# Kernel optimization log

Hardware: AMD Instinct MI355X
Metric: run time of the kernel (lower is better)

## Reference

```python
import jax, jax.numpy as jnp
import numpy as np

# dims
B, T, E = 2, 4096, 512
H = 8
DH = E // H            # 64 per-head dim
DEPTH = 4
NHASH = 4              # n_hashes
BUCKET = 64            # bucket_size
NB = T // BUCKET       # n_buckets = 64 (even)
VOCAB, NCLASS = 32000, 10
FF = 4 * E
MASK_VAL = -1e9        # causal mask value
SELF_VAL = -5e4        # TOKEN_SELF_ATTN_VALUE


def layer_norm(x, g, b):
    m = jnp.mean(x, axis=-1, keepdims=True)
    v = jnp.var(x, axis=-1, keepdims=True)
    return (x - m) * jax.lax.rsqrt(v + 1e-5) * g + b


def lsh_attention(x, wqk, wv, wo, bo, rot):
    """Reformer LSH causal self-attention (eval mode, shared QK, n_hashes rounds)."""
    qk = (x @ wqk).reshape(B, T, H, DH).transpose(0, 2, 1, 3).reshape(B * H, T, DH)
    v = (x @ wv).reshape(B, T, H, DH).transpose(0, 2, 1, 3).reshape(B * H, T, DH)
    b = B * H
    # --- hash: random rotations -> bucket ids per hash round ---
    rotated = jnp.einsum('btf,fhi->bhti', qk, rot)             # (b, NHASH, T, NB//2)
    rotated = jnp.concatenate([rotated, -rotated], axis=-1)    # (b, NHASH, T, NB)
    buckets = jnp.argmax(rotated, axis=-1)                     # (b, NHASH, T)
    buckets = buckets + (jnp.arange(NHASH) * NB)[None, :, None]
    buckets = buckets.reshape(b, NHASH * T)
    # --- stable sort by (bucket, time) ---
    ticker = jnp.arange(NHASH * T)
    bt = buckets * T + (ticker % T)
    sticker = jnp.argsort(bt, axis=-1)                         # sort permutation
    undo_sort = jnp.argsort(sticker, axis=-1)
    st = sticker % T                                           # original time index of sorted slot
    sqk = jnp.take_along_axis(qk, st[..., None], axis=1)
    sv = jnp.take_along_axis(v, st[..., None], axis=1)
    # --- chunk into buckets, attend to own + previous chunk ---
    C = NHASH * NB                                             # number of chunks
    bq_t = st.reshape(b, C, BUCKET)
    bqk = sqk.reshape(b, C, BUCKET, DH)
    bv = sv.reshape(b, C, BUCKET, DH)
    bq = bqk
    bk = bqk / jnp.maximum(jnp.linalg.norm(bqk, axis=-1, keepdims=True), 1e-12)
    look = lambda t: jnp.concatenate([t, jnp.roll(t, 1, axis=1)], axis=2)
    bk, bvl, bkv_t = look(bk), look(bv), look(bq_t)
    dots = jnp.einsum('bcie,bcje->bcij', bq, bk) * (DH ** -0.5)  # (b, C, BUCKET, 2*BUCKET)
    causal = bq_t[:, :, :, None] < bkv_t[:, :, None, :]
    dots = jnp.where(causal, MASK_VAL, dots)
    self_m = bq_t[:, :, :, None] == bkv_t[:, :, None, :]
    dots = jnp.where(self_m, SELF_VAL, dots)
    lse = jax.nn.logsumexp(dots, axis=-1, keepdims=True)
    probs = jnp.exp(dots - lse)
    so = jnp.einsum('bcij,bcje->bcie', probs, bvl).reshape(b, NHASH * T, DH)
    slogits = lse.reshape(b, NHASH * T)
    # --- unsort and combine hash rounds via logsumexp weights ---
    o = jnp.take_along_axis(so, undo_sort[..., None], axis=1).reshape(b, NHASH, T, DH)
    logits = jnp.take_along_axis(slogits, undo_sort, axis=1).reshape(b, NHASH, T, 1)
    w = jnp.exp(logits - jax.nn.logsumexp(logits, axis=1, keepdims=True))
    out = jnp.sum(o * w, axis=1)                               # (b, T, DH)
    out = out.reshape(B, H, T, DH).transpose(0, 2, 1, 3).reshape(B, T, E)
    return out @ wo + bo


def feed_forward(x, w1, b1, w2, b2):
    return jax.nn.gelu(x @ w1 + b1, approximate=False) @ w2 + b2


def setup_inputs() -> dict:
    key = jax.random.key(0)
    ks = jax.random.split(key, 12)
    n = lambda k, s: (0.02 * jax.random.normal(k, s)).astype(jnp.float32)
    return {
        'x': jax.random.randint(ks[0], (B, T), 0, VOCAB),
        'tok_emb': n(ks[1], (VOCAB, E)),
        'pos_emb': n(ks[2], (T, E)),
        'rotations': jax.random.normal(ks[3], (DEPTH, DH, NHASH, NB // 2), dtype=jnp.float32),
        'ln1_g': jnp.ones((DEPTH, E), jnp.float32), 'ln1_b': jnp.zeros((DEPTH, E), jnp.float32),
        'w_qk': n(ks[4], (DEPTH, E, E)), 'w_v': n(ks[5], (DEPTH, E, E)),
        'w_o': n(ks[6], (DEPTH, E, E)), 'b_o': jnp.zeros((DEPTH, E), jnp.float32),
        'ln2_g': jnp.ones((DEPTH, E), jnp.float32), 'ln2_b': jnp.zeros((DEPTH, E), jnp.float32),
        'w_ff1': n(ks[7], (DEPTH, E, FF)), 'b_ff1': jnp.zeros((DEPTH, FF), jnp.float32),
        'w_ff2': n(ks[8], (DEPTH, FF, E)), 'b_ff2': jnp.zeros((DEPTH, E), jnp.float32),
        'w_final': n(ks[9], (E, NCLASS)), 'b_final': jnp.zeros((NCLASS,), jnp.float32),
    }


def reference(x, tok_emb, pos_emb, rotations, ln1_g, ln1_b, w_qk, w_v, w_o, b_o,
              ln2_g, ln2_b, w_ff1, b_ff1, w_ff2, b_ff2, w_final, b_final):
    h = tok_emb[x] + pos_emb[None, :, :]
    # reversible sequence: y1 = x1 + attn(ln(x2)); y2 = x2 + ff(ln(y1))
    x1, x2 = h, h
    for d in range(DEPTH):
        x1 = x1 + lsh_attention(layer_norm(x2, ln1_g[d], ln1_b[d]),
                                w_qk[d], w_v[d], w_o[d], b_o[d], rotations[d])
        x2 = x2 + feed_forward(layer_norm(x1, ln2_g[d], ln2_b[d]),
                               w_ff1[d], b_ff1[d], w_ff2[d], b_ff2[d])
    h = 0.5 * (x1 + x2)
    pooled = jnp.mean(h, axis=1)          # pooling == 'avg'
    return pooled @ w_final + b_final
```

## Files before the change

### kernel.cpp

```cpp
#include <hip/hip_runtime.h>
#include <hip/hip_bf16.h>
#include <math.h>

#define B_      2
#define T_      4096
#define E_      512
#define H_      8
#define DH_     64
#define DEPTH_  4
#define NHASH_  4
#define BUCKET_ 64
#define NB_     64
#define NB2_    32
#define C_      (NHASH_*NB_)
#define BH_     (B_*H_)
#define NT_     (NHASH_*T_)
#define FF_     2048
#define NCLASS_ 10
#define MASKV   (-1e9f)
#define SELFV   (-5e4f)

typedef __attribute__((ext_vector_type(8))) short short8;
typedef __attribute__((ext_vector_type(4))) float f32x4;

__device__ __forceinline__ void gload_lds16(const void* g, void* l) {
    __builtin_amdgcn_global_load_lds(
        (const __attribute__((address_space(1))) void*)g,
        (__attribute__((address_space(3))) void*)l,
        16, 0, 0);
}

__device__ __forceinline__ unsigned pk2(float a, float b) {
    __hip_bfloat16 ha = __float2bfloat16(a), hb = __float2bfloat16(b);
    unsigned short ua = *(unsigned short*)&ha, ub = *(unsigned short*)&hb;
    return (unsigned)ua | ((unsigned)ub << 16);
}

__global__ __launch_bounds__(128) void k_embed(const int* __restrict__ x, const float* __restrict__ tok,
                                               const float* __restrict__ pos, float* __restrict__ x1,
                                               float* __restrict__ x2)
{
    int bt = blockIdx.x;
    int t  = bt & (T_ - 1);
    int id = x[bt];
    float4 tv = ((const float4*)(tok + (size_t)id * E_))[threadIdx.x];
    float4 pv = ((const float4*)(pos + (size_t)t * E_))[threadIdx.x];
    float4 hv = make_float4(tv.x + pv.x, tv.y + pv.y, tv.z + pv.z, tv.w + pv.w);
    ((float4*)(x1 + (size_t)bt * E_))[threadIdx.x] = hv;
    ((float4*)(x2 + (size_t)bt * E_))[threadIdx.x] = hv;
}

template<bool LO>
__global__ __launch_bounds__(128) void k_ln(const float* __restrict__ in, const float* __restrict__ g,
                                            const float* __restrict__ b, __hip_bfloat16* __restrict__ out,
                                            __hip_bfloat16* __restrict__ outlo)
{
    int row = blockIdx.x, tid = threadIdx.x;
    float4 v = ((const float4*)(in + (size_t)row * E_))[tid];
    float s = v.x + v.y + v.z + v.w;
    float q = v.x * v.x + v.y * v.y + v.z * v.z + v.w * v.w;
#pragma unroll
    for (int d = 1; d < 64; d <<= 1) { s += __shfl_xor(s, d); q += __shfl_xor(q, d); }
    __shared__ float red[4];
    int w = tid >> 6;
    if ((tid & 63) == 0) { red[w * 2] = s; red[w * 2 + 1] = q; }
    __syncthreads();
    s = red[0] + red[2]; q = red[1] + red[3];
    float mean = s * (1.0f / E_);
    float var  = q * (1.0f / E_) - mean * mean;
    float rstd = rsqrtf(var + 1e-5f);
    float4 gv = ((const float4*)g)[tid];
    float4 bv = ((const float4*)b)[tid];
    float o0 = (v.x - mean) * rstd * gv.x + bv.x;
    float o1 = (v.y - mean) * rstd * gv.y + bv.y;
    float o2 = (v.z - mean) * rstd * gv.z + bv.z;
    float o3 = (v.w - mean) * rstd * gv.w + bv.w;
    __hip_bfloat16* op = out + (size_t)row * E_ + tid * 4;
    __hip_bfloat16 h0 = __float2bfloat16(o0), h1 = __float2bfloat16(o1);
    __hip_bfloat16 h2 = __float2bfloat16(o2), h3 = __float2bfloat16(o3);
    op[0] = h0; op[1] = h1; op[2] = h2; op[3] = h3;
    if (LO) {
        __hip_bfloat16* lp = outlo + (size_t)row * E_ + tid * 4;
        lp[0] = __float2bfloat16(o0 - __bfloat162float(h0));
        lp[1] = __float2bfloat16(o1 - __bfloat162float(h1));
        lp[2] = __float2bfloat16(o2 - __bfloat162float(h2));
        lp[3] = __float2bfloat16(o3 - __bfloat162float(h3));
    }
}

template<bool SPLIT>
__global__ __launch_bounds__(256) void k_wprep(const float* __restrict__ W, __hip_bfloat16* __restrict__ WT,
                                               __hip_bfloat16* __restrict__ WTlo, int K, int N)
{
    __shared__ float tile[32][33];
    size_t lofs = (size_t)blockIdx.z * K * N;
    W  += lofs;
    WT += lofs;
    if (SPLIT) WTlo += lofs;
    int n0 = blockIdx.x * 32, k0 = blockIdx.y * 32;
    int tx = threadIdx.x & 31, ty = threadIdx.x >> 5;
#pragma unroll
    for (int i = 0; i < 4; ++i) {
        int k = ty + i * 8;
        tile[k][tx] = W[(size_t)(k0 + k) * N + n0 + tx];
    }
    __syncthreads();
#pragma unroll
    for (int i = 0; i < 4; ++i) {
        int n = ty + i * 8;
        float v = tile[tx][n];
        __hip_bfloat16 hv = __float2bfloat16(v);
        WT[(size_t)(n0 + n) * K + k0 + tx] = hv;
        if (SPLIT)
            WTlo[(size_t)(n0 + n) * K + k0 + tx] = __float2bfloat16(v - __bfloat162float(hv));
    }
}

__global__ __launch_bounds__(256) void k_rotprep(const float* __restrict__ rot,
                                                 __hip_bfloat16* __restrict__ rhs,
                                                 __hip_bfloat16* __restrict__ rls)
{
    int d = blockIdx.x;
    rot += (size_t)d * 64 * 128;
    rhs += (size_t)d * 8192;
    rls += (size_t)d * 8192;
    int tid = threadIdx.x;
    for (int idx = tid; idx < 128 * 64; idx += 256) {
        int row = idx >> 6, f = idx & 63;
        float v = rot[(size_t)f * 128 + row];
        __hip_bfloat16 hv = __float2bfloat16(v);
        __hip_bfloat16 lv = __float2bfloat16(v - __bfloat162float(hv));
        int b = f >> 3;
        int off = row * 64 + (((b ^ (row & 7)) << 3) | (f & 7));
        rhs[off] = hv;
        rls[off] = lv;
    }
}

__device__ __forceinline__ float geluf(float x) {
    float ax = fabsf(x) * 0.70710678118654752f;
    float t  = __builtin_amdgcn_rcpf(1.0f + 0.3275911f * ax);
    float poly = t * (0.254829592f + t * (-0.284496736f + t * (1.421413741f +
                 t * (-1.453152027f + t * 1.061405429f))));
    float e = __expf(-ax * ax);
    float erfax = 1.0f - poly * e;
    float erfx = copysignf(erfax, x);
    return 0.5f * x * (1.0f + erfx);
}

template<int OUTK, int BIAS, int TM>
__global__ __launch_bounds__(256) void k_mgemm(const __hip_bfloat16* __restrict__ A,
                                               const __hip_bfloat16* __restrict__ WT,
                                               const float* __restrict__ bias, void* __restrict__ Cout,
                                               int N, int K, int nbnShift)
{
    constexpr int MF = TM / 32;
    constexpr int ABYTES = TM * 128;
    __shared__ __align__(16) char smem[2 * ABYTES + 32768];
    char* BbBase = smem + 2 * ABYTES;

    int tid = threadIdx.x;
    int lane = tid & 63, wv = tid >> 6, w = wv;
    int nwg = gridDim.x;
    int bid = blockIdx.x;
    int swz = (bid & 7) * (nwg >> 3) + (bid >> 3);
    int nmask = (1 << nbnShift) - 1;
    int m0 = (swz >> nbnShift) * TM, n0 = (swz & nmask) * 128;
    int wm = (w >> 1) * (TM / 2), wn = (w & 1) * 64;

    const __hip_bfloat16* aSg[MF];
    int aDd[MF];
#pragma unroll
    for (int g = 0; g < MF; ++g) {
        int d = (wv + g * 4) * 64 + lane;
        int row = d >> 3, slot = d & 7;
        int c = (slot - ((row >> 1) & 7)) & 7;
        aSg[g] = A + (size_t)(m0 + row) * K + c * 8;
        aDd[g] = d * 16;
    }
    const __hip_bfloat16* bSg[4];
    int bDd[4];
#pragma unroll
    for (int g = 0; g < 4; ++g) {
        int d = (wv + g * 4) * 64 + lane;
        int row = d >> 3, slot = d & 7;
        int c = (slot - ((row >> 1) & 7)) & 7;
        bSg[g] = WT + (size_t)(n0 + row) * K + c * 8;
        bDd[g] = d * 16;
    }

    int cch = lane >> 4;
    int aoff[MF][2], boff[4][2];
#pragma unroll
    for (int f = 0; f < MF; ++f) {
        int ar = wm + f * 16 + (lane & 15);
        int rot = (ar >> 1) & 7;
#pragma unroll
        for (int h = 0; h < 2; ++h)
            aoff[f][h] = ar * 128 + (((h * 4 + cch) + rot) & 7) * 16;
    }
#pragma unroll
    for (int f = 0; f < 4; ++f) {
        int br = wn + f * 16 + (lane & 15);
        int rot = (br >> 1) & 7;
#pragma unroll
        for (int h = 0; h < 2; ++h)
            boff[f][h] = br * 128 + (((h * 4 + cch) + rot) & 7) * 16;
    }

    f32x4 acc[MF][4];
#pragma unroll
    for (int i = 0; i < MF; ++i)
#pragma unroll
        for (int j = 0; j < 4; ++j) acc[i][j] = (f32x4){0.f, 0.f, 0.f, 0.f};

    const int NS = K >> 6;
    {
#pragma unroll
        for (int g = 0; g < MF; ++g) gload_lds16(aSg[g], smem + aDd[g]);
#pragma unroll
        for (int g = 0; g < 4; ++g)  gload_lds16(bSg[g], BbBase + bDd[g]);
    }
    __syncthreads();
    for (int s = 0; s < NS; ++s) {
        int cur = s & 1;
        if (s + 1 < NS) {
            int nb = cur ^ 1;
            int kk = (s + 1) * 64;
            char* Abn = smem + nb * ABYTES;
            char* Bbn = BbBase + nb * 16384;
#pragma unroll
            for (int g = 0; g < MF; ++g) gload_lds16(aSg[g] + kk, Abn + aDd[g]);
#pragma unroll
            for (int g = 0; g < 4; ++g)  gload_lds16(bSg[g] + kk, Bbn + bDd[g]);
        }
        const char* Ab = smem + cur * ABYTES;
        const char* Bb = BbBase + cur * 16384;
#pragma unroll
        for (int h = 0; h < 2; ++h) {
            short8 af[MF], bfr[4];
#pragma unroll
            for (int f = 0; f < MF; ++f) af[f] = *(const short8*)(Ab + aoff[f][h]);
#pragma unroll
            for (int f = 0; f < 4; ++f)  bfr[f] = *(const short8*)(Bb + boff[f][h]);
#pragma unroll
            for (int i = 0; i < MF; ++i)
#pragma unroll
                for (int j = 0; j < 4; ++j)
                    acc[i][j] = __builtin_amdgcn_mfma_f32_16x16x32_bf16(af[i], bfr[j], acc[i][j], 0, 0, 0);
        }
        __syncthreads();
    }

    int g = lane >> 4;
    if (OUTK == 2 || OUTK == 3) {
        unsigned short* Ot = (unsigned short*)smem;
#pragma unroll
        for (int i = 0; i < MF; ++i) {
#pragma unroll
            for (int j = 0; j < 4; ++j) {
                int col = wn + j * 16 + (lane & 15);
                float bv = BIAS ? bias[n0 + col] : 0.f;
#pragma unroll
                for (int q = 0; q < 4; ++q) {
                    int row = wm + i * 16 + g * 4 + q;
                    float vv = acc[i][j][q] + bv;
                    if (OUTK == 2) vv = geluf(vv);
                    __hip_bfloat16 hv = __float2bfloat16(vv);
                    Ot[row * 128 + (((col >> 3) ^ (row & 7)) << 3) + (col & 7)] = *(unsigned short*)&hv;
                }
            }
        }
        __syncthreads();
#pragma unroll
        for (int u = 0; u < TM / 16; ++u) {
            int f = u * 256 + tid;
            int row = f >> 4, cblk = f & 15;
            uint4 v = *(const uint4*)(Ot + row * 128 + ((cblk ^ (row & 7)) << 3));
            if (OUTK == 2) {
                *(uint4*)((__hip_bfloat16*)Cout + (size_t)(m0 + row) * N + n0 + cblk * 8) = v;
            } else {
                int mrow = m0 + row;
                int t = mrow & (T_ - 1), bI = mrow >> 12;
                int col = n0 + cblk * 8;
                int h = col >> 6, fin = col & 63;
                *(uint4*)((__hip_bfloat16*)Cout + ((size_t)(bI * H_ + h) * T_ + t) * 64 + fin) = v;
            }
        }
    } else {
        float* Ot = (float*)smem;
        float* Cb = (float*)Cout;
#pragma unroll
        for (int i = 0; i < MF; ++i) {
#pragma unroll
            for (int j = 0; j < 4; ++j) {
                int col = wn + j * 16 + (lane & 15);
#pragma unroll
                for (int q = 0; q < 4; ++q) {
                    int row = wm + i * 16 + g * 4 + q;
                    Ot[row * 128 + (((col >> 2) ^ (row & 7)) << 2) + (col & 3)] = acc[i][j][q];
                }
            }
        }
        __syncthreads();
#pragma unroll
        for (int u = 0; u < 8; ++u) {
            int f = u * 256 + tid;
            int row = f >> 5, c4 = f & 31;
            float4 v = *(const float4*)(Ot + row * 128 + ((c4 ^ (row & 7)) << 2));
            if (BIAS) {
                float4 bv = *(const float4*)(bias + n0 + c4 * 4);
                v.x += bv.x; v.y += bv.y; v.z += bv.z; v.w += bv.w;
            }
            float* cp = Cb + (size_t)(m0 + row) * N + n0 + c4 * 4;
            float4 old = *(const float4*)cp;
            v.x += old.x; v.y += old.y; v.z += old.z; v.w += old.w;
            *(float4*)cp = v;
        }
    }
}

#define STG_A(buf, kt, h) \
    gload_lds16(aSrc + (size_t)((h) * 128) * K + (kt) * 64,      smem + (buf) * 32768 + (h) * 16384 + tid * 16); \
    gload_lds16(aSrc + (size_t)((h) * 128 + 64) * K + (kt) * 64, smem + (buf) * 32768 + (h) * 16384 + 8192 + tid * 16);
#define STG_B(buf, kt, h) \
    gload_lds16(bSrc + (size_t)((h) * 128) * K + (kt) * 64,      smem + 65536 + (buf) * 32768 + (h) * 16384 + tid * 16); \
    gload_lds16(bSrc + (size_t)((h) * 128 + 64) * K + (kt) * 64, smem + 65536 + (buf) * 32768 + (h) * 16384 + 8192 + tid * 16);

#define PHASE8(buf, MH, NH, RA, RB, STAGE, GATE) do {                                             \
    const char* Ab_ = smem + (buf) * 32768;                                                       \
    const char* Bb_ = smem + 65536 + (buf) * 32768;                                               \
    STAGE                                                                                         \
    if (RA) {                                                                                     \
        _Pragma("unroll")                                                                         \
        for (int mf = 0; mf < 4; ++mf) {                                                          \
            int row = arow + (MH) * 128 + mf * 16;                                                \
            aF[mf][0] = *(const short8*)(Ab_ + row * 128 + sw0);                                  \
            aF[mf][1] = *(const short8*)(Ab_ + row * 128 + sw1);                                  \
        }                                                                                         \
    }                                                                                             \
    if (RB) {                                                                                     \
        _Pragma("unroll")                                                                         \
        for (int nf = 0; nf < 2; ++nf) {                                                          \
            int row = brow + (NH) * 128 + nf * 16;                                                \
            bF[nf][0] = *(const short8*)(Bb_ + row * 128 + sw0);                                  \
            bF[nf][1] = *(const short8*)(Bb_ + row * 128 + sw1);                                  \
        }                                                                                         \
    }                                                                                             \
    GATE                                                                                          \
    __builtin_amdgcn_s_barrier();                                                                 \
    asm volatile("s_waitcnt lgkmcnt(0)" ::: "memory");                                            \
    __builtin_amdgcn_sched_barrier(0);                                                            \
    __builtin_amdgcn_s_setprio(1);                                                                \
    _Pragma("unroll")                                                                             \
    for (int mf = 0; mf < 4; ++mf)                                                                \
        _Pragma("unroll")                                                                         \
        for (int nf = 0; nf < 2; ++nf) {                                                          \
            acc[MH][NH][mf][nf] = __builtin_amdgcn_mfma_f32_16x16x32_bf16(aF[mf][0], bF[nf][0], acc[MH][NH][mf][nf], 0, 0, 0); \
            acc[MH][NH][mf][nf] = __builtin_amdgcn_mfma_f32_16x16x32_bf16(aF[mf][1], bF[nf][1], acc[MH][NH][mf][nf], 0, 0, 0); \
        }                                                                                         \
    __builtin_amdgcn_s_setprio(0);                                                                \
    __builtin_amdgcn_s_barrier();                                                                 \
} while (0)

__global__ __launch_bounds__(512, 2) void k_gemm256_gelu(const __hip_bfloat16* __restrict__ A,
                                                         const __hip_bfloat16* __restrict__ WT,
                                                         const float* __restrict__ bias,
                                                         __hip_bfloat16* __restrict__ Cout,
                                                         int N, int K, int nShift)
{
    __shared__ __align__(16) char smem[131072];
    const int NT = K >> 6;
    int tid = threadIdx.x;
    int lane = tid & 63, w = tid >> 6;
    int lane7 = lane & 7, cch = lane >> 4;
    int nwg = gridDim.x;
    int bid = blockIdx.x;
    int swz = (bid & 7) * (nwg >> 3) + (bid >> 3);
    int m0 = (swz >> nShift) * 256;
    int n0 = (swz & ((1 << nShift) - 1)) * 256;

    int rstg = tid >> 3;
    int kcstg = (tid & 7) ^ (rstg & 7);
    const __hip_bfloat16* aSrc = A  + (size_t)(m0 + rstg) * K + kcstg * 8;
    const __hip_bfloat16* bSrc = WT + (size_t)(n0 + rstg) * K + kcstg * 8;

    int arow = (w >> 2) * 64 + (lane & 15);
    int brow = (w & 3) * 32 + (lane & 15);
    int sw0 = (cch ^ lane7) << 4;
    int sw1 = ((4 + cch) ^ lane7) << 4;

    f32x4 acc[2][2][4][2];
#pragma unroll
    for (int a2 = 0; a2 < 2; ++a2)
#pragma unroll
        for (int b2 = 0; b2 < 2; ++b2)
#pragma unroll
            for (int c2 = 0; c2 < 4; ++c2)
#pragma unroll
                for (int d2 = 0; d2 < 2; ++d2) acc[a2][b2][c2][d2] = (f32x4){0.f, 0.f, 0.f, 0.f};

    short8 aF[4][2], bF[2][2];

    STG_A(0, 0, 0) STG_A(0, 0, 1) STG_B(0, 0, 0) STG_B(0, 0, 1)
    if (NT > 1) { STG_A(1, 1, 0) STG_B(1, 1, 1) }
    if (NT > 1) asm volatile("s_waitcnt vmcnt(4)" ::: "memory");
    else        asm volatile("s_waitcnt vmcnt(0)" ::: "memory");
    __builtin_amdgcn_s_barrier();

    for (int t = 0; t < NT; ++t) {
        int buf = t & 1;
        PHASE8(buf, 0, 0, 1, 1, { if (t + 1 < NT) { STG_A(buf ^ 1, t + 1, 1) } }, {});
        PHASE8(buf, 0, 1, 0, 1, { if (t + 1 < NT) { STG_B(buf ^ 1, t + 1, 0) } }, {});
        PHASE8(buf, 1, 1, 1, 0, { if (t + 2 < NT) { STG_A(buf, t + 2, 0) } }, {});
        PHASE8(buf, 1, 0, 0, 1, { if (t + 2 < NT) { STG_B(buf, t + 2, 1) } },
               { if (t + 2 < NT)      asm volatile("s_waitcnt vmcnt(4)" ::: "memory");
                 else if (t + 1 < NT) asm volatile("s_waitcnt vmcnt(0)" ::: "memory"); });
    }

    unsigned short* Ot = (unsigned short*)smem;
    int g = lane >> 4;
#pragma unroll
    for (int mh = 0; mh < 2; ++mh)
#pragma unroll
        for (int nh = 0; nh < 2; ++nh)
#pragma unroll
            for (int nf = 0; nf < 2; ++nf) {
                int coll = nh * 128 + (w & 3) * 32 + nf * 16 + (lane & 15);
                float bv = bias[n0 + coll];
#pragma unroll
                for (int mf = 0; mf < 4; ++mf)
#pragma unroll
                    for (int q = 0; q < 4; ++q) {
                        int rowl = mh * 128 + (w >> 2) * 64 + mf * 16 + g * 4 + q;
                        float vv = geluf(acc[mh][nh][mf][nf][q] + bv);
                        __hip_bfloat16 hv = __float2bfloat16(vv);
                        Ot[rowl * 256 + ((((coll >> 4) ^ (rowl & 7)) << 4) | (coll & 15))] = *(unsigned short*)&hv;
                    }
            }
    __syncthreads();
#pragma unroll
    for (int u = 0; u < 16; ++u) {
        int f = u * 512 + tid;
        int rowl = f >> 5, c16 = f & 31;
        uint4 v = *(const uint4*)(Ot + rowl * 256 + ((((c16 >> 1) ^ (rowl & 7)) << 4) | ((c16 & 1) << 3)));
        *(uint4*)(Cout + (size_t)(m0 + rowl) * N + n0 + c16 * 8) = v;
    }
}
#undef PHASE8
#undef STG_A
#undef STG_B

__global__ __launch_bounds__(256) void k_mgemm_qk(const __hip_bfloat16* __restrict__ Ah,
                                                  const __hip_bfloat16* __restrict__ Al,
                                                  const __hip_bfloat16* __restrict__ Bh,
                                                  const __hip_bfloat16* __restrict__ Bl,
                                                  float* __restrict__ Cout)
{
    __shared__ __align__(16) char smem[49152];
    const int N = 512, K = 512;
    int tid = threadIdx.x;
    int lane = tid & 63, w = tid >> 6;
    int nwg = gridDim.x;
    int bid = blockIdx.x;
    int swz = (bid & 7) * (nwg >> 3) + (bid >> 3);
    int m0 = (swz >> 2) * 64, n0 = (swz & 3) * 128;
    int wm = (w >> 1) * 32, wn = (w & 1) * 64;

    int r0 = tid >> 2, s0 = tid & 3;
    int c0 = (s0 - (r0 >> 1)) & 3;
    int r1 = r0 + 64;
    int c1 = (s0 - (r1 >> 1)) & 3;
    const __hip_bfloat16* ahS  = Ah + (size_t)(m0 + r0) * K + c0 * 8;
    const __hip_bfloat16* alS  = Al + (size_t)(m0 + r0) * K + c0 * 8;
    const __hip_bfloat16* bhS0 = Bh + (size_t)(n0 + r0) * K + c0 * 8;
    const __hip_bfloat16* bhS1 = Bh + (size_t)(n0 + r1) * K + c1 * 8;
    const __hip_bfloat16* blS0 = Bl + (size_t)(n0 + r0) * K + c0 * 8;
    const __hip_bfloat16* blS1 = Bl + (size_t)(n0 + r1) * K + c1 * 8;

    int cch = lane >> 4;
    int aoff[2], boff[4];
#pragma unroll
    for (int f = 0; f < 2; ++f) {
        int ar = wm + f * 16 + (lane & 15);
        aoff[f] = ar * 32 + (((cch + (ar >> 1)) & 3) * 8);
    }
#pragma unroll
    for (int f = 0; f < 4; ++f) {
        int br = wn + f * 16 + (lane & 15);
        boff[f] = br * 32 + (((cch + (br >> 1)) & 3) * 8);
    }

    f32x4 acc[2][4];
#pragma unroll
    for (int i = 0; i < 2; ++i)
#pragma unroll
        for (int j = 0; j < 4; ++j) acc[i][j] = (f32x4){0.f, 0.f, 0.f, 0.f};

#define QK_STAGE(buf, kk)                                                     \
    { char* bb = smem + (buf) * 24576;                                        \
      gload_lds16(ahS  + (kk), bb + tid * 16);                                \
      gload_lds16(alS  + (kk), bb + 4096  + tid * 16);                        \
      gload_lds16(bhS0 + (kk), bb + 8192  + tid * 16);                        \
      gload_lds16(bhS1 + (kk), bb + 12288 + tid * 16);                        \
      gload_lds16(blS0 + (kk), bb + 16384 + tid * 16);                        \
      gload_lds16(blS1 + (kk), bb + 20480 + tid * 16); }

    QK_STAGE(0, 0)
    __syncthreads();
    const int NS = K >> 5;
    for (int s = 0; s < NS; ++s) {
        int cur = s & 1;
        if (s + 1 < NS) QK_STAGE(cur ^ 1, (s + 1) * 32)
        const __hip_bfloat16* AhB = (const __hip_bfloat16*)(smem + cur * 24576);
        const __hip_bfloat16* AlB = (const __hip_bfloat16*)(smem + cur * 24576 + 4096);
        const __hip_bfloat16* BhB = (const __hip_bfloat16*)(smem + cur * 24576 + 8192);
        const __hip_bfloat16* BlB = (const __hip_bfloat16*)(smem + cur * 24576 + 16384);
        short8 afh[2], afl[2], bfh[4], bfl[4];
#pragma unroll
        for (int f = 0; f < 2; ++f) {
            afh[f] = *(const short8*)(AhB + aoff[f]);
            afl[f] = *(const short8*)(AlB + aoff[f]);
        }
#pragma unroll
        for (int f = 0; f < 4; ++f) {
            bfh[f] = *(const short8*)(BhB + boff[f]);
            bfl[f] = *(const short8*)(BlB + boff[f]);
        }
#pragma unroll
        for (int i = 0; i < 2; ++i)
#pragma unroll
            for (int j = 0; j < 4; ++j) {
                acc[i][j] = __builtin_amdgcn_mfma_f32_16x16x32_bf16(afh[i], bfh[j], acc[i][j], 0, 0, 0);
                acc[i][j] = __builtin_amdgcn_mfma_f32_16x16x32_bf16(afh[i], bfl[j], acc[i][j], 0, 0, 0);
                acc[i][j] = __builtin_amdgcn_mfma_f32_16x16x32_bf16(afl[i], bfh[j], acc[i][j], 0, 0, 0);
            }
        __syncthreads();
    }
#undef QK_STAGE

    int g = lane >> 4;
    float* Ot = (float*)smem;
#pragma unroll
    for (int i = 0; i < 2; ++i) {
#pragma unroll
        for (int j = 0; j < 4; ++j) {
            int col = wn + j * 16 + (lane & 15);
#pragma unroll
            for (int q = 0; q < 4; ++q) {
                int row = wm + i * 16 + g * 4 + q;
                Ot[row * 128 + (((col >> 2) ^ (row & 7)) << 2) + (col & 3)] = acc[i][j][q];
            }
        }
    }
    __syncthreads();
#pragma unroll
    for (int u = 0; u < 8; ++u) {
        int f = u * 256 + tid;
        int row = f >> 5, c4 = f & 31;
        float4 v = *(const float4*)(Ot + row * 128 + ((c4 ^ (row & 7)) << 2));
        *(float4*)(Cout + (size_t)(m0 + row) * N + n0 + c4 * 4) = v;
    }
}

__global__ __launch_bounds__(256) void k_hash(const float* __restrict__ qk,
                                              const __hip_bfloat16* __restrict__ rhs,
                                              const __hip_bfloat16* __restrict__ rls,
                                              unsigned char* __restrict__ bkt,
                                              __hip_bfloat16* __restrict__ qh,
                                              __hip_bfloat16* __restrict__ kh)
{
    __shared__ __align__(16) char smem[65536];
    char* RH = smem;
    char* RL = smem + 16384;
    char* QH = smem + 32768;
    char* QL = smem + 49152;
    int tid = threadIdx.x, lane = tid & 63, wv = tid >> 6;
    int bh = blockIdx.x, tc = blockIdx.y;
    int bI = bh >> 3, h = bh & 7;

#pragma unroll
    for (int it = 0; it < 4; ++it) {
        gload_lds16((const char*)rhs + it * 4096 + tid * 16, RH + it * 4096 + tid * 16);
        gload_lds16((const char*)rls + it * 4096 + tid * 16, RL + it * 4096 + tid * 16);
    }

    {
        int t = tid >> 1, half = tid & 1;
        int tg = tc * 128 + t;
        const float4* qsrc = (const float4*)(qk + ((size_t)(bI * T_ + tg)) * E_ + h * DH_ + half * 32);
        float4 q4[8];
        float n2 = 0.f;
#pragma unroll
        for (int j = 0; j < 8; ++j) {
            q4[j] = qsrc[j];
            n2 += q4[j].x * q4[j].x + q4[j].y * q4[j].y + q4[j].z * q4[j].z + q4[j].w * q4[j].w;
        }
        n2 += __shfl_xor(n2, 1);
        float sc = 0.125f / fmaxf(sqrtf(n2), 1e-12f);
        float qv[32];
#pragma unroll
        for (int j = 0; j < 8; ++j) {
            qv[4 * j] = q4[j].x; qv[4 * j + 1] = q4[j].y; qv[4 * j + 2] = q4[j].z; qv[4 * j + 3] = q4[j].w;
        }
        unsigned short hb[32], lb[32], kb[32];
#pragma unroll
        for (int j = 0; j < 32; ++j) {
            __hip_bfloat16 hv = __float2bfloat16(qv[j]);
            __hip_bfloat16 lv = __float2bfloat16(qv[j] - __bfloat162float(hv));
            __hip_bfloat16 kv = __float2bfloat16(qv[j] * sc);
            hb[j] = *(unsigned short*)&hv; lb[j] = *(unsigned short*)&lv; kb[j] = *(unsigned short*)&kv;
        }
        size_t ro = ((size_t)bh * T_ + tg) * 64 + half * 32;
        uint4* qdst = (uint4*)(qh + ro);
        uint4* kdst = (uint4*)(kh + ro);
#pragma unroll
        for (int j = 0; j < 4; ++j) {
            qdst[j] = *(uint4*)&hb[8 * j];
            kdst[j] = *(uint4*)&kb[8 * j];
        }
#pragma unroll
        for (int j = 0; j < 4; ++j) {
            int b = half * 4 + j;
            int xo = t * 128 + ((b ^ (t & 7)) << 4);
            *(uint4*)(QH + xo) = *(uint4*)&hb[8 * j];
            *(uint4*)(QL + xo) = *(uint4*)&lb[8 * j];
        }
    }
    __syncthreads();

#pragma unroll
    for (int sub = 0; sub < 2; ++sub) {
        int tl = wv * 32 + sub * 16 + (lane & 15);
        int g = lane >> 4;
        short8 qfh0 = *(const short8*)(QH + tl * 128 + ((g ^ (tl & 7)) << 4));
        short8 qfh1 = *(const short8*)(QH + tl * 128 + (((4 + g) ^ (tl & 7)) << 4));
        short8 qfl0 = *(const short8*)(QL + tl * 128 + ((g ^ (tl & 7)) << 4));
        short8 qfl1 = *(const short8*)(QL + tl * 128 + (((4 + g) ^ (tl & 7)) << 4));
        f32x4 sacc[8];
#pragma unroll
        for (int kt = 0; kt < 8; ++kt) sacc[kt] = (f32x4){0.f, 0.f, 0.f, 0.f};
#pragma unroll
        for (int kt = 0; kt < 8; ++kt) {
            int row = kt * 16 + (lane & 15);
            short8 rh0 = *(const short8*)(RH + row * 128 + ((g ^ (row & 7)) << 4));
            short8 rh1 = *(const short8*)(RH + row * 128 + (((4 + g) ^ (row & 7)) << 4));
            short8 rl0 = *(const short8*)(RL + row * 128 + ((g ^ (row & 7)) << 4));
            short8 rl1 = *(const short8*)(RL + row * 128 + (((4 + g) ^ (row & 7)) << 4));
            sacc[kt] = __builtin_amdgcn_mfma_f32_16x16x32_bf16(rh0, qfh0, sacc[kt], 0, 0, 0);
            sacc[kt] = __builtin_amdgcn_mfma_f32_16x16x32_bf16(rh1, qfh1, sacc[kt], 0, 0, 0);
            sacc[kt] = __builtin_amdgcn_mfma_f32_16x16x32_bf16(rl0, qfh0, sacc[kt], 0, 0, 0);
            sacc[kt] = __builtin_amdgcn_mfma_f32_16x16x32_bf16(rl1, qfh1, sacc[kt], 0, 0, 0);
            sacc[kt] = __builtin_amdgcn_mfma_f32_16x16x32_bf16(rh0, qfl0, sacc[kt], 0, 0, 0);
            sacc[kt] = __builtin_amdgcn_mfma_f32_16x16x32_bf16(rh1, qfl1, sacc[kt], 0, 0, 0);
        }
#pragma unroll
        for (int rd = 0; rd < 4; ++rd) {
            float bv = -3.0e38f; int bi = 0;
#pragma unroll
            for (int kp = 0; kp < 2; ++kp) {
#pragma unroll
                for (int rr = 0; rr < 4; ++rr) {
                    int i = kp * 16 + g * 4 + rr;
                    float v = sacc[rd * 2 + kp][rr];
                    if (v > bv) { bv = v; bi = i; }
                }
            }
#pragma unroll
            for (int kp = 0; kp < 2; ++kp) {
#pragma unroll
                for (int rr = 0; rr < 4; ++rr) {
                    int i = 32 + kp * 16 + g * 4 + rr;
                    float v = -sacc[rd * 2 + kp][rr];
                    if (v > bv) { bv = v; bi = i; }
                }
            }
#pragma unroll
            for (int dlt = 16; dlt <= 32; dlt <<= 1) {
                float ov = __shfl_xor(bv, dlt);
                int oi = __shfl_xor(bi, dlt);
                if (ov > bv || (ov == bv && oi < bi)) { bv = ov; bi = oi; }
            }
            if (g == 0)
                bkt[((size_t)(bh * NHASH_ + rd)) * T_ + tc * 128 + tl] = (unsigned char)bi;
        }
    }
}

__global__ __launch_bounds__(256) void k_sort(const unsigned char* __restrict__ bkt, int* __restrict__ st)
{
    __shared__ unsigned char bktL[T_];
    __shared__ unsigned short hist[256][66];
    __shared__ unsigned short qtot[4][64];
    __shared__ int qbase[4][64];
    int tid = threadIdx.x;
    int bhr = blockIdx.x;
    const unsigned char* src = bkt + (size_t)bhr * T_;
    ((uint4*)bktL)[tid] = ((const uint4*)src)[tid];
    uint4* h4 = (uint4*)&hist[0][0];
    for (int j = tid; j < 2112; j += 256) h4[j] = make_uint4(0, 0, 0, 0);
    __syncthreads();
    int base = tid * 16;
#pragma unroll
    for (int i = 0; i < 16; ++i) hist[tid][bktL[base + i]]++;
    __syncthreads();
    int b = tid & 63, qd = tid >> 6;
    int t0 = qd * 64;
    unsigned run = 0;
#pragma unroll 8
    for (int tt = 0; tt < 64; ++tt) {
        unsigned v = hist[t0 + tt][b];
        hist[t0 + tt][b] = (unsigned short)run;
        run += v;
    }
    qtot[qd][b] = (unsigned short)run;
    __syncthreads();
    if (tid < 64) {
        int c0 = qtot[0][tid], c1 = qtot[1][tid], c2 = qtot[2][tid], c3 = qtot[3][tid];
        int tot = c0 + c1 + c2 + c3;
        int pre = tot;
#pragma unroll
        for (int d = 1; d < 64; d <<= 1) { int o = __shfl_up(pre, d); if (tid >= d) pre += o; }
        int startb = pre - tot;
        qbase[0][tid] = startb;
        qbase[1][tid] = startb + c0;
        qbase[2][tid] = startb + c0 + c1;
        qbase[3][tid] = startb + c0 + c1 + c2;
    }
    __syncthreads();
    int* dst = st + (size_t)bhr * T_;
#pragma unroll
    for (int i = 0; i < 16; ++i) {
        int bb = bktL[base + i];
        int off = hist[tid][bb]++;
        dst[qbase[qd][bb] + off] = base + i;
    }
}

__global__ __launch_bounds__(256, 2) void k_attn(const __hip_bfloat16* __restrict__ qh,
                                                 const __hip_bfloat16* __restrict__ kh,
                                                 const __hip_bfloat16* __restrict__ vh,
                                                 const int* __restrict__ st,
                                                 __hip_bfloat16* __restrict__ o,
                                                 float* __restrict__ lg)
{
    __shared__ __align__(16) char smem[49664];
    char* KbB = smem;
    char* VtB = smem + 16384;
    char* PbB = smem + 32768;
    int*  kvt = (int*)(smem + 49152);
    unsigned short* ObU = (unsigned short*)smem;

    int tid = threadIdx.x;
    int lane = tid & 63;
    int g = lane >> 4;
    int wv = tid >> 6;
    int wq0 = wv * 16;

    int bid = blockIdx.x;
    int bh = ((bid & 7) << 1) | ((bid >> 3) & 1);
    int c  = bid >> 4;
    int rnd = c >> 6;
    int cp = (c + C_ - 1) & (C_ - 1);
    const size_t stB = (size_t)bh * NT_;

    if (tid < 128) {
        int cc = (tid < 64) ? c : cp;
        kvt[tid] = st[stB + (size_t)cc * 64 + (tid & 63)];
    }
    __syncthreads();

    {
        int k = tid >> 1, half = tid & 1;
        const uint4* src = (const uint4*)(kh + ((size_t)bh * T_ + kvt[k]) * 64 + half * 32);
#pragma unroll
        for (int j2 = 0; j2 < 4; ++j2) {
            uint4 a = src[j2];
            int blk = (half * 4 + j2) ^ (k & 7);
            *(uint4*)(KbB + k * 128 + blk * 16) = a;
        }
    }
    {
        int kp = tid & 63, dq = tid >> 6;
        const uint4* r0 = (const uint4*)(vh + ((size_t)bh * T_ + kvt[2 * kp]) * 64 + dq * 16);
        const uint4* r1 = (const uint4*)(vh + ((size_t)bh * T_ + kvt[2 * kp + 1]) * 64 + dq * 16);
        unsigned short va[16], vb2[16];
        *(uint4*)&va[0] = r0[0];  *(uint4*)&va[8] = r0[1];
        *(uint4*)&vb2[0] = r1[0]; *(uint4*)&vb2[8] = r1[1];
#pragma unroll
        for (int i = 0; i < 16; ++i) {
            int d = dq * 16 + i;
            unsigned wrd = (unsigned)va[i] | ((unsigned)vb2[i] << 16);
            *(unsigned*)(VtB + d * 256 + ((((kp >> 2) ^ i)) << 4) + ((kp & 3) << 2)) = wrd;
        }
    }
    int tq = kvt[wq0 + (lane & 15)];
    const __hip_bfloat16* qrow = qh + ((size_t)bh * T_ + tq) * 64;
    short8 qf0 = *(const short8*)(qrow + g * 8);
    short8 qf1 = *(const short8*)(qrow + 32 + g * 8);
    __syncthreads();

    f32x4 sacc[8];
#pragma unroll
    for (int kt = 0; kt < 8; ++kt) sacc[kt] = (f32x4){0.f, 0.f, 0.f, 0.f};
#pragma unroll
    for (int kt = 0; kt < 8; ++kt) {
        int row = kt * 16 + (lane & 15);
        short8 kf0 = *(const short8*)(KbB + row * 128 + (((g) ^ (row & 7)) << 4));
        short8 kf1 = *(const short8*)(KbB + row * 128 + (((4 + g) ^ (row & 7)) << 4));
        sacc[kt] = __builtin_amdgcn_mfma_f32_16x16x32_bf16(kf0, qf0, sacc[kt], 0, 0, 0);
        sacc[kt] = __builtin_amdgcn_mfma_f32_16x16x32_bf16(kf1, qf1, sacc[kt], 0, 0, 0);
    }

    float m = -3.0e38f;
#pragma unroll
    for (int kt = 0; kt < 8; ++kt) {
#pragma unroll
        for (int r = 0; r < 4; ++r) {
            int tk = kvt[kt * 16 + g * 4 + r];
            float dd = sacc[kt][r];
            dd = (tk > tq) ? MASKV : dd;
            dd = (tk == tq) ? SELFV : dd;
            sacc[kt][r] = dd;
            m = fmaxf(m, dd);
        }
    }
    m = fmaxf(m, __shfl_xor(m, 16));
    m = fmaxf(m, __shfl_xor(m, 32));
    float ssum = 0.f;
#pragma unroll
    for (int kt = 0; kt < 8; ++kt) {
        float p0 = __expf(sacc[kt][0] - m);
        float p1 = __expf(sacc[kt][1] - m);
        float p2 = __expf(sacc[kt][2] - m);
        float p3 = __expf(sacc[kt][3] - m);
        ssum += (p0 + p1) + (p2 + p3);
        uint2 wrd = make_uint2(pk2(p0, p1), pk2(p2, p3));
        int blk = (kt * 2 + (g >> 1)) ^ (lane & 15);
        *(uint2*)(PbB + (wq0 + (lane & 15)) * 256 + (blk << 4) + ((g & 1) << 3)) = wrd;
    }
    ssum += __shfl_xor(ssum, 16);
    ssum += __shfl_xor(ssum, 32);
    if (lane < 16)
        lg[((size_t)bh * T_ + tq) * 4 + rnd] = m + __logf(ssum);

    f32x4 pacc[4];
#pragma unroll
    for (int dt = 0; dt < 4; ++dt) pacc[dt] = (f32x4){0.f, 0.f, 0.f, 0.f};
#pragma unroll
    for (int s = 0; s < 4; ++s) {
        int xr = ((s * 4 + g) ^ (lane & 15)) << 4;
        short8 pf = *(const short8*)(PbB + (wq0 + (lane & 15)) * 256 + xr);
#pragma unroll
        for (int dt = 0; dt < 4; ++dt) {
            short8 vf = *(const short8*)(VtB + (dt * 16 + (lane & 15)) * 256 + xr);
            pacc[dt] = __builtin_amdgcn_mfma_f32_16x16x32_bf16(pf, vf, pacc[dt], 0, 0, 0);
        }
    }
    __syncthreads();

#pragma unroll
    for (int r = 0; r < 4; ++r) {
        float sr = __shfl(ssum, g * 4 + r);
        float inv = 1.0f / sr;
        int rowl = wq0 + g * 4 + r;
#pragma unroll
        for (int dt = 0; dt < 4; ++dt) {
            __hip_bfloat16 hv = __float2bfloat16(pacc[dt][r] * inv);
            ObU[rowl * 72 + dt * 16 + (lane & 15)] = *(unsigned short*)&hv;
        }
    }
    __syncthreads();

    {
        int rr = tid >> 2, seg = tid & 3;
        uint4 a = *(const uint4*)(ObU + rr * 72 + seg * 16);
        uint4 b = *(const uint4*)(ObU + rr * 72 + seg * 16 + 8);
        size_t jor = (size_t)bh * T_ + kvt[rr];
        uint4* dst = (uint4*)(o + jor * 256 + rnd * 64 + seg * 16);
        dst[0] = a; dst[1] = b;
    }
}

__global__ __launch_bounds__(256) void k_combine(const __hip_bfloat16* __restrict__ o,
                                                 const float* __restrict__ lg,
                                                 __hip_bfloat16* __restrict__ att)
{
    __shared__ float ws[H_][8];
    int bt = blockIdx.x;
    int bI = bt >> 12;
    int t  = bt & (T_ - 1);
    int tid = threadIdx.x;
    if (tid < H_) {
        size_t base = ((size_t)(bI * H_ + tid) * T_ + t);
        float4 L = *(const float4*)(lg + base * 4);
        float M = fmaxf(fmaxf(L.x, L.y), fmaxf(L.z, L.w));
        float w0 = __expf(L.x - M), w1 = __expf(L.y - M), w2 = __expf(L.z - M), w3 = __expf(L.w - M);
        float inv = 1.0f / (w0 + w1 + w2 + w3);
        ws[tid][0] = w0 * inv; ws[tid][1] = w1 * inv; ws[tid][2] = w2 * inv; ws[tid][3] = w3 * inv;
    }
    __syncthreads();
#pragma unroll
    for (int it = 0; it < 2; ++it) {
        int e = it * 256 + tid;
        int h = e >> 6, f = e & 63;
        const __hip_bfloat16* op = o + ((size_t)(bI * H_ + h) * T_ + t) * 256;
        float val = __bfloat162float(op[f])       * ws[h][0]
                  + __bfloat162float(op[64 + f])  * ws[h][1]
                  + __bfloat162float(op[128 + f]) * ws[h][2]
                  + __bfloat162float(op[192 + f]) * ws[h][3];
        att[(size_t)bt * E_ + e] = __float2bfloat16(val);
    }
}

__global__ __launch_bounds__(256) void k_pool1(const float* __restrict__ x1, const float* __restrict__ x2,
                                               float* __restrict__ part)
{
    int blk = blockIdx.x;
    int bI = blk >> 5, tc = blk & 31;
    int t0 = tc * 128;
    for (int e = threadIdx.x; e < E_; e += 256) {
        float s = 0.f;
        for (int t = t0; t < t0 + 128; ++t) {
            size_t idx = ((size_t)bI * T_ + t) * E_ + e;
            s += x1[idx] + x2[idx];
        }
        part[((size_t)bI * 32 + tc) * E_ + e] = s;
    }
}

__global__ __launch_bounds__(256) void k_final(const float* __restrict__ part, const float* __restrict__ wf,
                                               const float* __restrict__ bf, float* __restrict__ out)
{
    __shared__ float pooled[B_ * E_];
    int tid = threadIdx.x;
    for (int i = tid; i < B_ * E_; i += 256) {
        int bI = i >> 9, e = i & 511;
        float s = 0.f;
        for (int c2 = 0; c2 < 32; ++c2) s += part[((size_t)bI * 32 + c2) * E_ + e];
        pooled[i] = s * (0.5f / T_);
    }
    __syncthreads();
    if (tid < B_ * NCLASS_) {
        int bI = tid / NCLASS_, cl = tid % NCLASS_;
        float s = bf[cl];
        for (int e = 0; e < E_; ++e) s += pooled[bI * E_ + e] * wf[(size_t)e * NCLASS_ + cl];
        out[tid] = s;
    }
}

extern "C" void kernel_launch(void* const* d_in, const int* in_sizes, int n_in,
                              void* d_out, int out_size, void* d_ws, size_t ws_size,
                              hipStream_t stream)
{
    const int*   X    = (const int*)d_in[0];
    const float* TOK  = (const float*)d_in[1];
    const float* POS  = (const float*)d_in[2];
    const float* ROT  = (const float*)d_in[3];
    const float* LN1G = (const float*)d_in[4];
    const float* LN1B = (const float*)d_in[5];
    const float* WQK  = (const float*)d_in[6];
    const float* WV   = (const float*)d_in[7];
    const float* WO   = (const float*)d_in[8];
    const float* BO   = (const float*)d_in[9];
    const float* LN2G = (const float*)d_in[10];
    const float* LN2B = (const float*)d_in[11];
    const float* WF1  = (const float*)d_in[12];
    const float* BF1  = (const float*)d_in[13];
    const float* WF2  = (const float*)d_in[14];
    const float* BF2  = (const float*)d_in[15];
    const float* WFIN = (const float*)d_in[16];
    const float* BFIN = (const float*)d_in[17];

    float* ws = (float*)d_ws;
    const size_t S = (size_t)B_ * T_ * E_;
    float* x1   = ws;
    float* x2   = x1 + S;
    float* qkb  = x2 + S;
    float* vb   = qkb + S;
    float* bigf = vb + S;
    float* lgb  = bigf + 2 * S;
    float* part = lgb + (size_t)BH_ * NT_;
    __hip_bfloat16* lnbh  = (__hip_bfloat16*)(part + (size_t)B_ * 32 * E_);
    __hip_bfloat16* lnbl  = lnbh + S;
    __hip_bfloat16* attnb = lnbl + S;
    int*   stb  = (int*)(attnb + S);
    __hip_bfloat16* WTbase = (__hip_bfloat16*)(stb + (size_t)BH_ * NT_);
    __hip_bfloat16* big    = (__hip_bfloat16*)bigf;

    const size_t W55 = (size_t)512 * 512;
    const size_t WFF = (size_t)2048 * 512;
    __hip_bfloat16* WTqk_hi = WTbase;
    __hip_bfloat16* WTqk_lo = WTqk_hi + 4 * W55;
    __hip_bfloat16* WTv     = WTqk_lo + 4 * W55;
    __hip_bfloat16* WTo     = WTv     + 4 * W55;
    __hip_bfloat16* WTf1    = WTo     + 4 * W55;
    __hip_bfloat16* WTf2    = WTf1    + 4 * WFF;
    unsigned char*  bktb    = (unsigned char*)(WTf2 + 4 * WFF);
    __hip_bfloat16* qh      = (__hip_bfloat16*)(bktb + (size_t)BH_ * NHASH_ * T_);
    __hip_bfloat16* khb     = qh  + (size_t)BH_ * T_ * 64;
    __hip_bfloat16* vhb     = khb + (size_t)BH_ * T_ * 64;
    __hip_bfloat16* rswzh   = vhb + (size_t)BH_ * T_ * 64;
    __hip_bfloat16* rswzl   = rswzh + 4 * 8192;

    k_wprep<true ><<<dim3(16, 16, 4), 256, 0, stream>>>(WQK, WTqk_hi, WTqk_lo, 512, 512);
    k_wprep<false><<<dim3(16, 16, 4), 256, 0, stream>>>(WV, WTv, nullptr, 512, 512);
    k_wprep<false><<<dim3(16, 16, 4), 256, 0, stream>>>(WO, WTo, nullptr, 512, 512);
    k_wprep<false><<<dim3(64, 16, 4), 256, 0, stream>>>(WF1, WTf1, nullptr, 512, 2048);
    k_wprep<false><<<dim3(16, 64, 4), 256, 0, stream>>>(WF2, WTf2, nullptr, 2048, 512);
    k_rotprep<<<4, 256, 0, stream>>>(ROT, rswzh, rswzl);

    const int g512_64 = (512 / 128) * ((B_ * T_) / 64);
    const int gff1    = ((B_ * T_) / 256) * (FF_ / 256);

    k_embed<<<B_ * T_, 128, 0, stream>>>(X, TOK, POS, x1, x2);
    for (int d = 0; d < DEPTH_; ++d) {
        k_ln<true><<<B_ * T_, 128, 0, stream>>>(x2, LN1G + (size_t)d * E_, LN1B + (size_t)d * E_, lnbh, lnbl);
        k_mgemm_qk<<<g512_64, 256, 0, stream>>>(lnbh, lnbl, WTqk_hi + d * W55, WTqk_lo + d * W55, qkb);
        k_mgemm<3, 0, 64><<<g512_64, 256, 0, stream>>>(lnbh, WTv + d * W55, nullptr, vhb, 512, 512, 2);
        k_hash<<<dim3(BH_, T_ / 128), 256, 0, stream>>>(qkb, rswzh + d * 8192, rswzl + d * 8192,
                                                        bktb, qh, khb);
        k_sort<<<BH_ * NHASH_, 256, 0, stream>>>(bktb, stb);
        k_attn<<<BH_ * C_, 256, 0, stream>>>(qh, khb, vhb, stb, big, lgb);
        k_combine<<<B_ * T_, 256, 0, stream>>>(big, lgb, attnb);
        k_mgemm<1, 1, 64><<<g512_64, 256, 0, stream>>>(attnb, WTo + d * W55, BO + (size_t)d * E_, x1,
                                                       512, 512, 2);
        k_ln<false><<<B_ * T_, 128, 0, stream>>>(x1, LN2G + (size_t)d * E_, LN2B + (size_t)d * E_, lnbh, nullptr);
        k_gemm256_gelu<<<gff1, 512, 0, stream>>>(lnbh, WTf1 + d * WFF, BF1 + (size_t)d * FF_, big,
                                                 2048, 512, 3);
        k_mgemm<1, 1, 64><<<g512_64, 256, 0, stream>>>(big, WTf2 + d * WFF, BF2 + (size_t)d * E_, x2,
                                                       512, 2048, 2);
    }
    k_pool1<<<B_ * 32, 256, 0, stream>>>(x1, x2, part);
    k_final<<<1, 256, 0, stream>>>(part, WFIN, BFIN, (float*)d_out);
}
```

Before: 773.3 us.

## Retile split-bf16 QK GEMM to 64x64 tiles and shrink attention LDS

```diff
diff --git a/kernel.cpp b/kernel.cpp
--- a/kernel.cpp
+++ b/kernel.cpp
@@ -451,114 +451,117 @@
 #undef STG_A
 #undef STG_B
 
-__global__ __launch_bounds__(256) void k_mgemm_qk(const __hip_bfloat16* __restrict__ Ah,
-                                                  const __hip_bfloat16* __restrict__ Al,
-                                                  const __hip_bfloat16* __restrict__ Bh,
-                                                  const __hip_bfloat16* __restrict__ Bl,
-                                                  float* __restrict__ Cout)
-{
-    __shared__ __align__(16) char smem[49152];
+__global__ __launch_bounds__(256) void k_qk64(const __hip_bfloat16* __restrict__ Ah,
+                                              const __hip_bfloat16* __restrict__ Al,
+                                              const __hip_bfloat16* __restrict__ Bh,
+                                              const __hip_bfloat16* __restrict__ Bl,
+                                              float* __restrict__ Cout)
+{
     const int N = 512, K = 512;
+    __shared__ __align__(16) char smem[65536];
     int tid = threadIdx.x;
-    int lane = tid & 63, w = tid >> 6;
+    int lane = tid & 63, wv = tid >> 6;
     int nwg = gridDim.x;
     int bid = blockIdx.x;
     int swz = (bid & 7) * (nwg >> 3) + (bid >> 3);
-    int m0 = (swz >> 2) * 64, n0 = (swz & 3) * 128;
-    int wm = (w >> 1) * 32, wn = (w & 1) * 64;
-
-    int r0 = tid >> 2, s0 = tid & 3;
-    int c0 = (s0 - (r0 >> 1)) & 3;
-    int r1 = r0 + 64;
-    int c1 = (s0 - (r1 >> 1)) & 3;
-    const __hip_bfloat16* ahS  = Ah + (size_t)(m0 + r0) * K + c0 * 8;
-    const __hip_bfloat16* alS  = Al + (size_t)(m0 + r0) * K + c0 * 8;
-    const __hip_bfloat16* bhS0 = Bh + (size_t)(n0 + r0) * K + c0 * 8;
-    const __hip_bfloat16* bhS1 = Bh + (size_t)(n0 + r1) * K + c1 * 8;
-    const __hip_bfloat16* blS0 = Bl + (size_t)(n0 + r0) * K + c0 * 8;
-    const __hip_bfloat16* blS1 = Bl + (size_t)(n0 + r1) * K + c1 * 8;
+    int m0 = (swz >> 3) * 64, n0 = (swz & 7) * 64;
+    int wm = (wv >> 1) * 32, wn = (wv & 1) * 32;
+
+    const __hip_bfloat16* sAh[2]; const __hip_bfloat16* sAl[2];
+    const __hip_bfloat16* sBh[2]; const __hip_bfloat16* sBl[2];
+    int dOf[2];
+#pragma unroll
+    for (int g = 0; g < 2; ++g) {
+        int d = (wv + g * 4) * 64 + lane;
+        int row = d >> 3, slot = d & 7;
+        int c = (slot - ((row >> 1) & 7)) & 7;
+        dOf[g] = d * 16;
+        sAh[g] = Ah + (size_t)(m0 + row) * K + c * 8;
+        sAl[g] = Al + (size_t)(m0 + row) * K + c * 8;
+        sBh[g] = Bh + (size_t)(n0 + row) * K + c * 8;
+        sBl[g] = Bl + (size_t)(n0 + row) * K + c * 8;
+    }
 
     int cch = lane >> 4;
-    int aoff[2], boff[4];
+    int aoff[2][2], boff[2][2];
 #pragma unroll
     for (int f = 0; f < 2; ++f) {
         int ar = wm + f * 16 + (lane & 15);
-        aoff[f] = ar * 32 + (((cch + (ar >> 1)) & 3) * 8);
-    }
-#pragma unroll
-    for (int f = 0; f < 4; ++f) {
+        int rta = (ar >> 1) & 7;
         int br = wn + f * 16 + (lane & 15);
-        boff[f] = br * 32 + (((cch + (br >> 1)) & 3) * 8);
-    }
-
-    f32x4 acc[2][4];
+        int rtb = (br >> 1) & 7;
+#pragma unroll
+        for (int h = 0; h < 2; ++h) {
+            aoff[f][h] = ar * 128 + (((h * 4 + cch) + rta) & 7) * 16;
+            boff[f][h] = br * 128 + (((h * 4 + cch) + rtb) & 7) * 16;
+        }
+    }
+
+    f32x4 acc[2][2];
 #pragma unroll
     for (int i = 0; i < 2; ++i)
 #pragma unroll
-        for (int j = 0; j < 4; ++j) acc[i][j] = (f32x4){0.f, 0.f, 0.f, 0.f};
-
-#define QK_STAGE(buf, kk)                                                     \
-    { char* bb = smem + (buf) * 24576;                                        \
-      gload_lds16(ahS  + (kk), bb + tid * 16);                                \
-      gload_lds16(alS  + (kk), bb + 4096  + tid * 16);                        \
-      gload_lds16(bhS0 + (kk), bb + 8192  + tid * 16);                        \
-      gload_lds16(bhS1 + (kk), bb + 12288 + tid * 16);                        \
-      gload_lds16(blS0 + (kk), bb + 16384 + tid * 16);                        \
-      gload_lds16(blS1 + (kk), bb + 20480 + tid * 16); }
-
-    QK_STAGE(0, 0)
-    __syncthreads();
-    const int NS = K >> 5;
+        for (int j = 0; j < 2; ++j) acc[i][j] = (f32x4){0.f, 0.f, 0.f, 0.f};
+
+#define QK_STG(buf, kk)                                              \
+    { char* bb = smem + (buf) * 32768;                               \
+      _Pragma("unroll")                                              \
+      for (int g = 0; g < 2; ++g) {                                  \
+          gload_lds16(sAh[g] + (kk), bb + dOf[g]);                   \
+          gload_lds16(sAl[g] + (kk), bb + 8192  + dOf[g]);           \
+          gload_lds16(sBh[g] + (kk), bb + 16384 + dOf[g]);           \
+          gload_lds16(sBl[g] + (kk), bb + 24576 + dOf[g]);           \
+      } }
+
+    QK_STG(0, 0)
+    __syncthreads();
+    const int NS = K >> 6;
     for (int s = 0; s < NS; ++s) {
         int cur = s & 1;
-        if (s + 1 < NS) QK_STAGE(cur ^ 1, (s + 1) * 32)
-        const __hip_bfloat16* AhB = (const __hip_bfloat16*)(smem + cur * 24576);
-        const __hip_bfloat16* AlB = (const __hip_bfloat16*)(smem + cur * 24576 + 4096);
-        const __hip_bfloat16* BhB = (const __hip_bfloat16*)(smem + cur * 24576 + 8192);
-        const __hip_bfloat16* BlB = (const __hip_bfloat16*)(smem + cur * 24576 + 16384);
-        short8 afh[2], afl[2], bfh[4], bfl[4];
-#pragma unroll
-        for (int f = 0; f < 2; ++f) {
-            afh[f] = *(const short8*)(AhB + aoff[f]);
-            afl[f] = *(const short8*)(AlB + aoff[f]);
-        }
-#pragma unroll
-        for (int f = 0; f < 4; ++f) {
-            bfh[f] = *(const short8*)(BhB + boff[f]);
-            bfl[f] = *(const short8*)(BlB + boff[f]);
-        }
-#pragma unroll
-        for (int i = 0; i < 2; ++i)
-#pragma unroll
-            for (int j = 0; j < 4; ++j) {
-                acc[i][j] = __builtin_amdgcn_mfma_f32_16x16x32_bf16(afh[i], bfh[j], acc[i][j], 0, 0, 0);
-                acc[i][j] = __builtin_amdgcn_mfma_f32_16x16x32_bf16(afh[i], bfl[j], acc[i][j], 0, 0, 0);
-                acc[i][j] = __builtin_amdgcn_mfma_f32_16x16x32_bf16(afl[i], bfh[j], acc[i][j], 0, 0, 0);
+        if (s + 1 < NS) QK_STG(cur ^ 1, (s + 1) * 64)
+        const char* bb = smem + cur * 32768;
+#pragma unroll
+        for (int h = 0; h < 2; ++h) {
+            short8 afh[2], afl[2], bfh[2], bfl[2];
+#pragma unroll
+            for (int f = 0; f < 2; ++f) {
+                afh[f] = *(const short8*)(bb + aoff[f][h]);
+                afl[f] = *(const short8*)(bb + 8192  + aoff[f][h]);
+                bfh[f] = *(const short8*)(bb + 16384 + boff[f][h]);
+                bfl[f] = *(const short8*)(bb + 24576 + boff[f][h]);
             }
+#pragma unroll
+            for (int i = 0; i < 2; ++i)
+#pragma unroll
+                for (int j = 0; j < 2; ++j) {
+                    acc[i][j] = __builtin_amdgcn_mfma_f32_16x16x32_bf16(afh[i], bfh[j], acc[i][j], 0, 0, 0);
+                    acc[i][j] = __builtin_amdgcn_mfma_f32_16x16x32_bf16(afh[i], bfl[j], acc[i][j], 0, 0, 0);
+                    acc[i][j] = __builtin_amdgcn_mfma_f32_16x16x32_bf16(afl[i], bfh[j], acc[i][j], 0, 0, 0);
+                }
+        }
         __syncthreads();
     }
-#undef QK_STAGE
+#undef QK_STG
 
     int g = lane >> 4;
     float* Ot = (float*)smem;
 #pragma unroll
-    for (int i = 0; i < 2; ++i) {
-#pragma unroll
-        for (int j = 0; j < 4; ++j) {
+    for (int i = 0; i < 2; ++i)
+#pragma unroll
+        for (int j = 0; j < 2; ++j) {
             int col = wn + j * 16 + (lane & 15);
 #pragma unroll
             for (int q = 0; q < 4; ++q) {
                 int row = wm + i * 16 + g * 4 + q;
-                Ot[row * 128 + (((col >> 2) ^ (row & 7)) << 2) + (col & 3)] = acc[i][j][q];
+                Ot[row * 64 + (((col >> 2) ^ (row & 7)) << 2) + (col & 3)] = acc[i][j][q];
             }
         }
-    }
-    __syncthreads();
-#pragma unroll
-    for (int u = 0; u < 8; ++u) {
+    __syncthreads();
+#pragma unroll
+    for (int u = 0; u < 4; ++u) {
         int f = u * 256 + tid;
-        int row = f >> 5, c4 = f & 31;
-        float4 v = *(const float4*)(Ot + row * 128 + ((c4 ^ (row & 7)) << 2));
+        int row = f >> 4, c4 = f & 15;
+        float4 v = *(const float4*)(Ot + row * 64 + ((c4 ^ (row & 7)) << 2));
         *(float4*)(Cout + (size_t)(m0 + row) * N + n0 + c4 * 4) = v;
     }
 }
@@ -737,18 +740,18 @@
     }
 }
 
-__global__ __launch_bounds__(256, 2) void k_attn(const __hip_bfloat16* __restrict__ qh,
+__global__ __launch_bounds__(256, 4) void k_attn(const __hip_bfloat16* __restrict__ qh,
                                                  const __hip_bfloat16* __restrict__ kh,
                                                  const __hip_bfloat16* __restrict__ vh,
                                                  const int* __restrict__ st,
                                                  __hip_bfloat16* __restrict__ o,
                                                  float* __restrict__ lg)
 {
-    __shared__ __align__(16) char smem[49664];
+    __shared__ __align__(16) char smem[33280];
     char* KbB = smem;
     char* VtB = smem + 16384;
-    char* PbB = smem + 32768;
-    int*  kvt = (int*)(smem + 49152);
+    char* PbB = smem;
+    int*  kvt = (int*)(smem + 32768);
     unsigned short* ObU = (unsigned short*)smem;
 
     int tid = threadIdx.x;
@@ -827,6 +830,7 @@
     }
     m = fmaxf(m, __shfl_xor(m, 16));
     m = fmaxf(m, __shfl_xor(m, 32));
+    __syncthreads();
     float ssum = 0.f;
 #pragma unroll
     for (int kt = 0; kt < 8; ++kt) {
@@ -1011,12 +1015,13 @@
     k_rotprep<<<4, 256, 0, stream>>>(ROT, rswzh, rswzl);
 
     const int g512_64 = (512 / 128) * ((B_ * T_) / 64);
+    const int gqk     = ((B_ * T_) / 64) * (512 / 64);
     const int gff1    = ((B_ * T_) / 256) * (FF_ / 256);
 
     k_embed<<<B_ * T_, 128, 0, stream>>>(X, TOK, POS, x1, x2);
     for (int d = 0; d < DEPTH_; ++d) {
         k_ln<true><<<B_ * T_, 128, 0, stream>>>(x2, LN1G + (size_t)d * E_, LN1B + (size_t)d * E_, lnbh, lnbl);
-        k_mgemm_qk<<<g512_64, 256, 0, stream>>>(lnbh, lnbl, WTqk_hi + d * W55, WTqk_lo + d * W55, qkb);
+        k_qk64<<<gqk, 256, 0, stream>>>(lnbh, lnbl, WTqk_hi + d * W55, WTqk_lo + d * W55, qkb);
         k_mgemm<3, 0, 64><<<g512_64, 256, 0, stream>>>(lnbh, WTv + d * W55, nullptr, vhb, 512, 512, 2);
         k_hash<<<dim3(BH_, T_ / 128), 256, 0, stream>>>(qkb, rswzh + d * 8192, rswzl + d * 8192,
                                                         bktb, qh, khb);
```

After: 756.0 us (median of 2 runs). -2.2%, faster.
